# Performance work log

Hardware: AMD Instinct MI355X
Metric: run time of the kernel (lower is better)

The kernel has to match this reference:

```python
import jax, jax.numpy as jnp
import numpy as np

SCALE_BASE = 512.0
GAMMA = 0.96875

def xpos(x, downscale=False):
    # x: (B, L, d). XPOS = rotary embedding with exponential position-dependent scale.
    B, L, d = x.shape
    half = d // 2
    scale_vec = (jnp.arange(0, d, 2, dtype=jnp.float32) + 0.4 * d) / (1.4 * d)  # (half,)
    pos = jnp.arange(L, dtype=jnp.float32)
    scale = scale_vec[None, :] ** (pos[:, None] / SCALE_BASE)  # (L, half)
    if downscale:
        scale = 1.0 / scale
    inv_freq = 1.0 / (10000.0 ** (jnp.arange(half, dtype=jnp.float32) / half))
    sinusoid = pos[:, None] * inv_freq[None, :]  # (L, half)
    sin_s = jnp.repeat(jnp.sin(sinusoid) * scale, 2, axis=-1)  # duplicate_interleave -> (L, d)
    cos_s = jnp.repeat(jnp.cos(sinusoid) * scale, 2, axis=-1)
    x1, x2 = x[..., ::2], x[..., 1::2]
    rot = jnp.stack((-x2, x1), axis=-1).reshape(x.shape)  # rotate_every_two
    return x * cos_s + rot * sin_s

def decay_mask(L, gamma):
    n = jnp.arange(L)[:, None]
    m = jnp.arange(L)[None, :]
    diff = n - m
    expo = jnp.where(diff >= 0, diff, 0).astype(jnp.float32)
    return jnp.where(diff >= 0, gamma ** expo, 0.0)  # (L, L) causal decay

def setup_inputs() -> dict:
    key = jax.random.key(0)
    kx, kq, kk, kv = jax.random.split(key, 4)
    B, L, H = 4, 2048, 1024
    hs = 1024  # head_size == v_dim
    X = jax.random.normal(kx, (B, L, H), dtype=jnp.float32)
    W_Q = jax.random.normal(kq, (H, hs), dtype=jnp.float32) / H
    W_K = jax.random.normal(kk, (H, hs), dtype=jnp.float32) / H
    W_V = jax.random.normal(kv, (H, hs), dtype=jnp.float32) / H
    return {"X": X, "W_Q": W_Q, "W_K": W_K, "W_V": W_V}

def reference(X, W_Q, W_K, W_V):
    L = X.shape[1]
    Q = xpos(X @ W_Q)
    K = xpos(X @ W_K, downscale=True)
    V = X @ W_V
    D = decay_mask(L, GAMMA)
    ret = jnp.einsum('bnd,bmd->bnm', Q, K) * D[None]  # (B, L, L)
    return ret @ V
```

## Files before the change

### kernel.cpp

```cpp
#include <hip/hip_runtime.h>
#include <cmath>

typedef __attribute__((ext_vector_type(8))) short short8;
typedef __attribute__((ext_vector_type(4))) short short4v;
typedef __attribute__((ext_vector_type(16))) float floatx16;
typedef __attribute__((ext_vector_type(4))) float float4v;
typedef unsigned short ushort_t;

#define LSEQ   2048
#define DMODEL 1024
#define BM 128
#define BN 128
#define BK 64
#define TPAD 136

#define L2GAMMA (-0.045803595f)
#define L2E4_512 (0.0259525632f)

__device__ __forceinline__ ushort_t f2b(float x) {
    union { float f; unsigned u; } v; v.f = x;
    unsigned r = v.u + 0x7fffu + ((v.u >> 16) & 1u);
    return (ushort_t)(r >> 16);
}

#define GLOAD_LDS16(gptr, lptr)                                                     \
    __builtin_amdgcn_global_load_lds(                                               \
        (const __attribute__((address_space(1))) unsigned int*)(gptr),              \
        (__attribute__((address_space(3))) unsigned int*)(lptr), 16, 0, 0)

#define MFMA_B16 __builtin_amdgcn_mfma_f32_32x32x16_bf16
#define MFMA16   __builtin_amdgcn_mfma_f32_16x16x32_bf16

__device__ __forceinline__ void gemm_core(
    const ushort_t* __restrict__ Ag, int lda, int aRow0,
    const ushort_t* __restrict__ Bg, int ldb, int bRow0,
    int kDepth, ushort_t* As, ushort_t* Bs, floatx16 acc[2][2])
{
    const int tid  = threadIdx.x;
    const int wave = tid >> 6, lane = tid & 63;
    const int wm = wave >> 1, wn = wave & 1;
    const int l31 = lane & 31, half = lane >> 5;
    const int srow = lane >> 3;
    const int scol = ((lane & 7) ^ srow) * 8;

    const ushort_t* ap[4];
    const ushort_t* bp[4];
    #pragma unroll
    for (int L = 0; L < 4; ++L) {
        int r = (wave * 4 + L) * 8 + srow;
        ap[L] = Ag + (size_t)(aRow0 + r) * lda + scol;
        bp[L] = Bg + (size_t)(bRow0 + r) * ldb + scol;
    }
    const int ldst = (lane >> 3) * BK + (lane & 7) * 8;

    for (int k0 = 0; k0 < kDepth; k0 += BK) {
        __syncthreads();
        #pragma unroll
        for (int L = 0; L < 4; ++L) {
            GLOAD_LDS16(ap[L], As + (wave * 4 + L) * (8 * BK) + ldst);
            GLOAD_LDS16(bp[L], Bs + (wave * 4 + L) * (8 * BK) + ldst);
            ap[L] += BK; bp[L] += BK;
        }
        __syncthreads();

        #pragma unroll
        for (int ks = 0; ks < 4; ++ks) {
            const int ch = ((ks * 2 + half) ^ (l31 & 7)) * 8;
            short8 a0 = *(const short8*)(As + (wm * 64      + l31) * BK + ch);
            short8 a1 = *(const short8*)(As + (wm * 64 + 32 + l31) * BK + ch);
            short8 b0 = *(const short8*)(Bs + (wn * 64      + l31) * BK + ch);
            short8 b1 = *(const short8*)(Bs + (wn * 64 + 32 + l31) * BK + ch);
            acc[0][0] = MFMA_B16(a0, b0, acc[0][0], 0, 0, 0);
            acc[0][1] = MFMA_B16(a0, b1, acc[0][1], 0, 0, 0);
            acc[1][0] = MFMA_B16(a1, b0, acc[1][0], 0, 0, 0);
            acc[1][1] = MFMA_B16(a1, b1, acc[1][1], 0, 0, 0);
        }
    }
}

__global__ __launch_bounds__(256) void xpos_table_kernel(float2* __restrict__ T)
{
    int idx = blockIdx.x * 256 + threadIdx.x;
    int l = idx & 2047;
    int p = (idx >> 11) & 511;
    int mode = idx >> 20;
    float sv = (2.0f * (float)p + 409.6f) * (1.0f / 1433.6f);
    float coeff = log2f(sv) * (1.0f / 512.0f) + L2GAMMA;
    float invf = exp2f(-(float)p * L2E4_512);
    float lf = (float)l;
    float s, c;
    sincosf(lf * invf, &s, &c);
    float g = exp2f((mode == 0 ? lf : -lf) * coeff);
    T[idx] = make_float2(c * g, s * g);
}

__global__ __launch_bounds__(256) void cast_x_kernel(
    const float4* __restrict__ X, short4v* __restrict__ Xb, int n4)
{
    int i = blockIdx.x * 256 + threadIdx.x;
    if (i < n4) {
        float4 v = X[i];
        short4v o;
        o.x = (short)f2b(v.x); o.y = (short)f2b(v.y);
        o.z = (short)f2b(v.z); o.w = (short)f2b(v.w);
        Xb[i] = o;
    }
}

__global__ __launch_bounds__(256) void wtrans_kernel(
    const float* __restrict__ Wq, const float* __restrict__ Wk,
    const float* __restrict__ Wv, ushort_t* __restrict__ Wt)
{
    const float* W = blockIdx.z == 0 ? Wq : blockIdx.z == 1 ? Wk : Wv;
    ushort_t* O = Wt + (size_t)blockIdx.z * (DMODEL * DMODEL);
    __shared__ float t[32][33];
    const int x = threadIdx.x & 31, y = (threadIdx.x >> 5) * 4;
    const int k0 = blockIdx.y * 32, n0 = blockIdx.x * 32;
    #pragma unroll
    for (int j = 0; j < 4; ++j)
        t[y + j][x] = W[(size_t)(k0 + y + j) * DMODEL + n0 + x];
    __syncthreads();
    #pragma unroll
    for (int j = 0; j < 4; ++j)
        O[(size_t)(n0 + y + j) * DMODEL + k0 + x] = f2b(t[x][y + j]);
}

__global__ __launch_bounds__(256) void qkv16_kernel(
    const ushort_t* __restrict__ Xb, const ushort_t* __restrict__ Wt,
    const float2* __restrict__ Tab,
    ushort_t* __restrict__ Q, ushort_t* __restrict__ Ko, ushort_t* __restrict__ Vt)
{
    __shared__ ushort_t smem[128 * TPAD];
    ushort_t* As = smem;
    ushort_t* Bs = smem + BM * BK;

    const int nwg = gridDim.x;
    const int orig = blockIdx.x;
    const int lin = (orig & 7) * (nwg >> 3) + (orig >> 3);
    const int inner = lin & 63;
    const int sup = lin >> 6;
    const int c = (sup % 3) * 8 + (inner & 7);
    const int r = (sup / 3) * 8 + (inner >> 3);
    const int mode = c >> 3;
    const int c0 = (c & 7) * BN;
    const int row0 = r * BM;

    const int tid = threadIdx.x;
    const int wave = tid >> 6, lane = tid & 63;
    const int wm = wave >> 1, wn = wave & 1;
    const int l15 = lane & 15, l4g = lane >> 4, l7 = lane & 7;

    const int srow = lane >> 3;
    const int scol = ((lane & 7) ^ srow) * 8;
    const char* gA = (const char*)Xb;
    const char* gB = (const char*)(Wt + (size_t)mode * (DMODEL * DMODEL));
    unsigned aoff[4], boff[4];
    #pragma unroll
    for (int L = 0; L < 4; ++L) {
        const int rr = (wave * 4 + L) * 8 + srow;
        aoff[L] = (unsigned)(((row0 + rr) * DMODEL + scol) * 2);
        boff[L] = (unsigned)(((c0 + rr) * DMODEL + scol) * 2);
    }
    const int ldst = srow * BK + (lane & 7) * 8;

    int aBase[2], bBase[2];
    #pragma unroll
    for (int h = 0; h < 2; ++h) {
        const int ch = ((h * 4 + l4g) ^ l7) * 8;
        aBase[h] = (wm * 64 + l15) * BK + ch;
        bBase[h] = (wn * 64 + l15) * BK + ch;
    }

    float4v acc[4][4] = {};

    for (int k0 = 0; k0 < DMODEL; k0 += BK) {
        __syncthreads();
        #pragma unroll
        for (int L = 0; L < 4; ++L) {
            GLOAD_LDS16(gA + aoff[L], As + (wave * 4 + L) * (8 * BK) + ldst);
            GLOAD_LDS16(gB + boff[L], Bs + (wave * 4 + L) * (8 * BK) + ldst);
            aoff[L] += 2 * BK; boff[L] += 2 * BK;
        }
        __syncthreads();

        #pragma unroll
        for (int h = 0; h < 2; ++h) {
            short8 a[4], b[4];
            #pragma unroll
            for (int f = 0; f < 4; ++f) {
                a[f] = *(const short8*)(As + aBase[h] + f * (16 * BK));
                b[f] = *(const short8*)(Bs + bBase[h] + f * (16 * BK));
            }
            #pragma unroll
            for (int fr = 0; fr < 4; ++fr)
                #pragma unroll
                for (int fc = 0; fc < 4; ++fc)
                    acc[fr][fc] = MFMA16(a[fr], b[fc], acc[fr][fc], 0, 0, 0);
        }
    }

    const int rB = row0 + wm * 64 + l4g * 4;
    const int cB = c0 + wn * 64 + l15;

    if (mode < 2) {
        ushort_t* O = (mode == 0) ? Q : Ko;
        const float2* Tm = Tab + (size_t)mode * (512 * 2048);
        #pragma unroll
        for (int fc = 0; fc < 4; ++fc) {
            const int col = cB + fc * 16;
            const float2* tp = Tm + ((size_t)(col >> 1) << 11);
            #pragma unroll
            for (int fr = 0; fr < 4; ++fr) {
                const int row = rB + fr * 16;
                const int l0 = row & 2047;
                float4 t01 = *(const float4*)(tp + l0);
                float4 t23 = *(const float4*)(tp + l0 + 2);
                float cs[8] = {t01.x, t01.y, t01.z, t01.w,
                               t23.x, t23.y, t23.z, t23.w};
                #pragma unroll
                for (int q = 0; q < 4; ++q) {
                    float v  = acc[fr][fc][q];
                    float pv = __shfl_xor(v, 1);
                    float cc = cs[2 * q], ss = cs[2 * q + 1];
                    float res = (lane & 1) ? fmaf(v, cc, pv * ss)
                                           : fmaf(v, cc, -pv * ss);
                    O[(size_t)(row + q) * DMODEL + col] = f2b(res);
                }
            }
        }
    } else {
        __syncthreads();
        #pragma unroll
        for (int fc = 0; fc < 4; ++fc)
            #pragma unroll
            for (int fr = 0; fr < 4; ++fr) {
                short4v pk;
                pk.x = (short)f2b(acc[fr][fc][0]);
                pk.y = (short)f2b(acc[fr][fc][1]);
                pk.z = (short)f2b(acc[fr][fc][2]);
                pk.w = (short)f2b(acc[fr][fc][3]);
                *(short4v*)(smem + (wn * 64 + fc * 16 + l15) * TPAD
                                 + wm * 64 + fr * 16 + l4g * 4) = pk;
            }
        __syncthreads();
        const int t = threadIdx.x;
        const int colV = c0 + (t >> 1);
        const int lhalf = (t & 1) * 64;
        const int b = row0 >> 11, lpos0 = (row0 & 2047) + lhalf;
        #pragma unroll
        for (int i = 0; i < 8; ++i) {
            short8 vv = *(const short8*)(smem + (t >> 1) * TPAD + lhalf + i * 8);
            *(short8*)(Vt + (size_t)b * (LSEQ * DMODEL)
                          + (size_t)colV * LSEQ + lpos0 + i * 8) = vv;
        }
    }
}

__global__ __launch_bounds__(256, 4) void score_kernel(
    const ushort_t* __restrict__ Q, const ushort_t* __restrict__ Kc,
    ushort_t* __restrict__ S)
{
    const int t = blockIdx.x, z = blockIdx.z;
    int bi, bj;
    if (t < 3) { bi = (t > 0); bj = t - (t > 0); }
    else { int u = t - 3; bi = 2 + u / 3; bj = bi - 2 + u % 3; }

    __shared__ ushort_t As[BM * BK], Bs[BN * BK];
    floatx16 acc[2][2] = {};
    const size_t zoff = (size_t)z * (LSEQ * DMODEL);
    gemm_core(Q + zoff, DMODEL, bi * BM, Kc + zoff, DMODEL, bj * BN,
              DMODEL, As, Bs, acc);

    const int wave = threadIdx.x >> 6, lane = threadIdx.x & 63;
    const int wm = wave >> 1, wn = wave & 1;
    const int l31 = lane & 31, half = lane >> 5;
    const int nBase = bi * BM + wm * 64 + 4 * half;
    const int mBase = bj * BN + wn * 64 + l31;
    ushort_t* Sz = S + (size_t)z * LSEQ * LSEQ;
    #pragma unroll
    for (int mi = 0; mi < 2; ++mi)
        #pragma unroll
        for (int ni = 0; ni < 2; ++ni) {
            int m = mBase + ni * 32;
            #pragma unroll
            for (int rg = 0; rg < 4; ++rg)
                #pragma unroll
                for (int q = 0; q < 4; ++q) {
                    int n = nBase + mi * 32 + 8 * rg + q;
                    Sz[(size_t)n * LSEQ + m] =
                        (m <= n) ? f2b(acc[mi][ni][rg * 4 + q]) : (ushort_t)0;
                }
        }
}

__global__ __launch_bounds__(256, 4) void av_kernel(
    const ushort_t* __restrict__ S, const ushort_t* __restrict__ Vt,
    float* __restrict__ Out)
{
    const int bx = blockIdx.x, bi = blockIdx.y, z = blockIdx.z;
    const int kLo = (bi >= 2) ? (bi - 2) * BM : 0;
    const int kW  = (bi + 1) * BM - kLo;
    __shared__ ushort_t As[BM * BK], Bs[BN * BK];
    floatx16 acc[2][2] = {};
    gemm_core(S + (size_t)z * LSEQ * LSEQ + kLo, LSEQ, bi * BM,
              Vt + (size_t)z * (LSEQ * DMODEL) + kLo, LSEQ, bx * BN,
              kW, As, Bs, acc);

    const int wave = threadIdx.x >> 6, lane = threadIdx.x & 63;
    const int wm = wave >> 1, wn = wave & 1;
    const int l31 = lane & 31, half = lane >> 5;
    const int rBase = bi * BM + wm * 64 + 4 * half;
    const int cBase = bx * BN + wn * 64 + l31;
    float* Oz = Out + (size_t)z * (LSEQ * DMODEL);
    #pragma unroll
    for (int mi = 0; mi < 2; ++mi)
        #pragma unroll
        for (int ni = 0; ni < 2; ++ni)
            #pragma unroll
            for (int rg = 0; rg < 4; ++rg)
                #pragma unroll
                for (int q = 0; q < 4; ++q)
                    Oz[(size_t)(rBase + mi * 32 + 8 * rg + q) * DMODEL
                       + cBase + ni * 32] = acc[mi][ni][rg * 4 + q];
}

extern "C" void kernel_launch(void* const* d_in, const int* in_sizes, int n_in,
                              void* d_out, int out_size, void* d_ws, size_t ws_size,
                              hipStream_t stream)
{
    const float* X  = (const float*)d_in[0];
    const float* Wq = (const float*)d_in[1];
    const float* Wk = (const float*)d_in[2];
    const float* Wv = (const float*)d_in[3];
    float* out = (float*)d_out;

    const size_t LH  = (size_t)LSEQ * DMODEL;
    const size_t WSZ = (size_t)DMODEL * DMODEL;
    const size_t SSZ = (size_t)LSEQ * LSEQ;
    const size_t TABN = (size_t)2 * 512 * 2048;

    size_t need4 = TABN * 8 + 2 * (3 * WSZ + 4 * (4 * LH + SSZ));
    const int bs = (ws_size >= need4) ? 4 : 1;

    float2* Tab = (float2*)d_ws;
    ushort_t* ws16 = (ushort_t*)(Tab + TABN);
    ushort_t* Wt = ws16;
    ushort_t* Xb = Wt + 3 * WSZ;
    ushort_t* Q  = Xb + (size_t)bs * LH;
    ushort_t* Kb = Q  + (size_t)bs * LH;
    ushort_t* Vt = Kb + (size_t)bs * LH;
    ushort_t* S  = Vt + (size_t)bs * LH;

    xpos_table_kernel<<<dim3(TABN / 256), 256, 0, stream>>>(Tab);
    wtrans_kernel<<<dim3(32, 32, 3), 256, 0, stream>>>(Wq, Wk, Wv, Wt);

    for (int p = 0; p < 4 / bs; ++p) {
        const float* Xp = X + (size_t)p * bs * LH;
        cast_x_kernel<<<dim3(bs * 2048), 256, 0, stream>>>(
            (const float4*)Xp, (short4v*)Xb, bs * (int)(LH / 4));
        qkv16_kernel<<<dim3(24 * bs * 16), 256, 0, stream>>>(
            Xb, Wt, Tab, Q, Kb, Vt);
        score_kernel<<<dim3(45, 1, bs), 256, 0, stream>>>(Q, Kb, S);
        av_kernel<<<dim3(8, 16, bs), 256, 0, stream>>>(S, Vt,
            out + (size_t)p * bs * LH);
    }
}
```

Before: 213.2 us.

## Double-buffer LDS tiles in GEMM cores to overlap global loads with MFMA

Converts the shared GEMM core and the QKV projection kernel to a two-stage LDS ping-pong. The next K-tile is loaded directly into LDS while MFMAs consume the current one, using vmcnt waits and raw barriers instead of two full __syncthreads per iteration. This targets global-load latency exposed between tiles. It doubles LDS per block and lowers the occupancy hint on the score and AV kernels from 4 to 2 waves per SIMD, which reduces latency hiding from concurrent workgroups.

```diff
diff --git a/kernel.cpp b/kernel.cpp
--- a/kernel.cpp
+++ b/kernel.cpp
@@ -51,30 +51,47 @@
         ap[L] = Ag + (size_t)(aRow0 + r) * lda + scol;
         bp[L] = Bg + (size_t)(bRow0 + r) * ldb + scol;
     }
-    const int ldst = (lane >> 3) * BK + (lane & 7) * 8;
-
-    for (int k0 = 0; k0 < kDepth; k0 += BK) {
-        __syncthreads();
-        #pragma unroll
-        for (int L = 0; L < 4; ++L) {
-            GLOAD_LDS16(ap[L], As + (wave * 4 + L) * (8 * BK) + ldst);
-            GLOAD_LDS16(bp[L], Bs + (wave * 4 + L) * (8 * BK) + ldst);
-            ap[L] += BK; bp[L] += BK;
-        }
-        __syncthreads();
+    const int ldst = srow * BK + (lane & 7) * 8;
+
+    const int nt = kDepth / BK;
+    #pragma unroll
+    for (int L = 0; L < 4; ++L) {
+        GLOAD_LDS16(ap[L], As + (wave * 4 + L) * (8 * BK) + ldst);
+        GLOAD_LDS16(bp[L], Bs + (wave * 4 + L) * (8 * BK) + ldst);
+        ap[L] += BK; bp[L] += BK;
+    }
+
+    for (int j = 0; j < nt; ++j) {
+        const int cur = (j & 1) * (BM * BK);
+        const int nxt = ((j + 1) & 1) * (BM * BK);
+        if (j + 1 < nt) {
+            #pragma unroll
+            for (int L = 0; L < 4; ++L) {
+                GLOAD_LDS16(ap[L], As + nxt + (wave * 4 + L) * (8 * BK) + ldst);
+                GLOAD_LDS16(bp[L], Bs + nxt + (wave * 4 + L) * (8 * BK) + ldst);
+                ap[L] += BK; bp[L] += BK;
+            }
+            asm volatile("s_waitcnt vmcnt(8)" ::: "memory");
+        } else {
+            asm volatile("s_waitcnt vmcnt(0)" ::: "memory");
+        }
+        __builtin_amdgcn_s_barrier();
+        asm volatile("" ::: "memory");
 
         #pragma unroll
         for (int ks = 0; ks < 4; ++ks) {
             const int ch = ((ks * 2 + half) ^ (l31 & 7)) * 8;
-            short8 a0 = *(const short8*)(As + (wm * 64      + l31) * BK + ch);
-            short8 a1 = *(const short8*)(As + (wm * 64 + 32 + l31) * BK + ch);
-            short8 b0 = *(const short8*)(Bs + (wn * 64      + l31) * BK + ch);
-            short8 b1 = *(const short8*)(Bs + (wn * 64 + 32 + l31) * BK + ch);
+            short8 a0 = *(const short8*)(As + cur + (wm * 64      + l31) * BK + ch);
+            short8 a1 = *(const short8*)(As + cur + (wm * 64 + 32 + l31) * BK + ch);
+            short8 b0 = *(const short8*)(Bs + cur + (wn * 64      + l31) * BK + ch);
+            short8 b1 = *(const short8*)(Bs + cur + (wn * 64 + 32 + l31) * BK + ch);
             acc[0][0] = MFMA_B16(a0, b0, acc[0][0], 0, 0, 0);
             acc[0][1] = MFMA_B16(a0, b1, acc[0][1], 0, 0, 0);
             acc[1][0] = MFMA_B16(a1, b0, acc[1][0], 0, 0, 0);
             acc[1][1] = MFMA_B16(a1, b1, acc[1][1], 0, 0, 0);
         }
+        asm volatile("" ::: "memory");
+        __builtin_amdgcn_s_barrier();
     }
 }
 
@@ -130,9 +147,9 @@
     const float2* __restrict__ Tab,
     ushort_t* __restrict__ Q, ushort_t* __restrict__ Ko, ushort_t* __restrict__ Vt)
 {
-    __shared__ ushort_t smem[128 * TPAD];
+    __shared__ ushort_t smem[32768];
     ushort_t* As = smem;
-    ushort_t* Bs = smem + BM * BK;
+    ushort_t* Bs = smem + 16384;
 
     const int nwg = gridDim.x;
     const int orig = blockIdx.x;
@@ -173,23 +190,38 @@
 
     float4v acc[4][4] = {};
 
-    for (int k0 = 0; k0 < DMODEL; k0 += BK) {
-        __syncthreads();
-        #pragma unroll
-        for (int L = 0; L < 4; ++L) {
-            GLOAD_LDS16(gA + aoff[L], As + (wave * 4 + L) * (8 * BK) + ldst);
-            GLOAD_LDS16(gB + boff[L], Bs + (wave * 4 + L) * (8 * BK) + ldst);
-            aoff[L] += 2 * BK; boff[L] += 2 * BK;
-        }
-        __syncthreads();
+    #pragma unroll
+    for (int L = 0; L < 4; ++L) {
+        GLOAD_LDS16(gA + aoff[L], As + (wave * 4 + L) * (8 * BK) + ldst);
+        GLOAD_LDS16(gB + boff[L], Bs + (wave * 4 + L) * (8 * BK) + ldst);
+        aoff[L] += 2 * BK; boff[L] += 2 * BK;
+    }
+
+    #pragma unroll 2
+    for (int k = 0; k < 16; ++k) {
+        const int cur = (k & 1) * (BM * BK);
+        const int nxt = ((k + 1) & 1) * (BM * BK);
+        if (k < 15) {
+            #pragma unroll
+            for (int L = 0; L < 4; ++L) {
+                GLOAD_LDS16(gA + aoff[L], As + nxt + (wave * 4 + L) * (8 * BK) + ldst);
+                GLOAD_LDS16(gB + boff[L], Bs + nxt + (wave * 4 + L) * (8 * BK) + ldst);
+                aoff[L] += 2 * BK; boff[L] += 2 * BK;
+            }
+            asm volatile("s_waitcnt vmcnt(8)" ::: "memory");
+        } else {
+            asm volatile("s_waitcnt vmcnt(0)" ::: "memory");
+        }
+        __builtin_amdgcn_s_barrier();
+        asm volatile("" ::: "memory");
 
         #pragma unroll
         for (int h = 0; h < 2; ++h) {
             short8 a[4], b[4];
             #pragma unroll
             for (int f = 0; f < 4; ++f) {
-                a[f] = *(const short8*)(As + aBase[h] + f * (16 * BK));
-                b[f] = *(const short8*)(Bs + bBase[h] + f * (16 * BK));
+                a[f] = *(const short8*)(As + cur + aBase[h] + f * (16 * BK));
+                b[f] = *(const short8*)(Bs + cur + bBase[h] + f * (16 * BK));
             }
             #pragma unroll
             for (int fr = 0; fr < 4; ++fr)
@@ -197,6 +229,8 @@
                 for (int fc = 0; fc < 4; ++fc)
                     acc[fr][fc] = MFMA16(a[fr], b[fc], acc[fr][fc], 0, 0, 0);
         }
+        asm volatile("" ::: "memory");
+        __builtin_amdgcn_s_barrier();
     }
 
     const int rB = row0 + wm * 64 + l4g * 4;
@@ -256,7 +290,7 @@
     }
 }
 
-__global__ __launch_bounds__(256, 4) void score_kernel(
+__global__ __launch_bounds__(256, 2) void score_kernel(
     const ushort_t* __restrict__ Q, const ushort_t* __restrict__ Kc,
     ushort_t* __restrict__ S)
 {
@@ -265,7 +299,7 @@
     if (t < 3) { bi = (t > 0); bj = t - (t > 0); }
     else { int u = t - 3; bi = 2 + u / 3; bj = bi - 2 + u % 3; }
 
-    __shared__ ushort_t As[BM * BK], Bs[BN * BK];
+    __shared__ ushort_t As[2 * BM * BK], Bs[2 * BN * BK];
     floatx16 acc[2][2] = {};
     const size_t zoff = (size_t)z * (LSEQ * DMODEL);
     gemm_core(Q + zoff, DMODEL, bi * BM, Kc + zoff, DMODEL, bj * BN,
@@ -293,14 +327,14 @@
         }
 }
 
-__global__ __launch_bounds__(256, 4) void av_kernel(
+__global__ __launch_bounds__(256, 2) void av_kernel(
     const ushort_t* __restrict__ S, const ushort_t* __restrict__ Vt,
     float* __restrict__ Out)
 {
     const int bx = blockIdx.x, bi = blockIdx.y, z = blockIdx.z;
     const int kLo = (bi >= 2) ? (bi - 2) * BM : 0;
     const int kW  = (bi + 1) * BM - kLo;
-    __shared__ ushort_t As[BM * BK], Bs[BN * BK];
+    __shared__ ushort_t As[2 * BM * BK], Bs[2 * BN * BK];
     floatx16 acc[2][2] = {};
     gemm_core(S + (size_t)z * LSEQ * LSEQ + kLo, LSEQ, bi * BM,
               Vt + (size_t)z * (LSEQ * DMODEL) + kLo, LSEQ, bx * BN,
```

After: 201.8 us. 1.06x faster.
